# Performance work log

Measured on AMD Instinct MI355X. Metric: run time of the kernel, lower is better.

## Reference

```python
import jax, jax.numpy as jnp
import numpy as np

N, H, V, MAX_STEPS = 256, 128, 64, 4

def setup_inputs() -> dict:
    key = jax.random.key(0)
    ks = jax.random.split(key, 16)
    def w(k, shape, fan_in):
        return jax.random.normal(k, shape, dtype=jnp.float32) / np.sqrt(fan_in)
    inp = {}
    inp['node_embeddings'] = jax.random.normal(ks[0], (N, H), dtype=jnp.float32)
    inp['skip_embeddings'] = jax.random.normal(ks[1], (N, N, H), dtype=jnp.float32)
    inp['Wx'] = w(ks[2], (H, 4 * H), H)
    inp['Wh'] = w(ks[3], (H, 4 * H), H)
    inp['b'] = jnp.zeros((4 * H,), jnp.float32)
    inp['Wxs'] = w(ks[4], (H, 4 * H), H)
    inp['Whs'] = w(ks[5], (H, 4 * H), H)
    inp['bs'] = jnp.zeros((4 * H,), jnp.float32)
    inp['Wb'] = w(ks[6], (2 * H, 2), 2 * H)
    inp['bb'] = jnp.zeros((2,), jnp.float32)
    inp['Wk'] = w(ks[7], (H, H), H)
    inp['bk'] = jnp.zeros((H,), jnp.float32)
    inp['Wq'] = w(ks[8], (2 * H, H), 2 * H)
    inp['bq'] = jnp.zeros((H,), jnp.float32)
    inp['Wl'] = w(ks[9], (2 * H, 1), 2 * H)
    inp['bl'] = jnp.zeros((1,), jnp.float32)
    inp['Wd'] = w(ks[10], (2 * H, V), 2 * H)
    inp['bd'] = jnp.zeros((V,), jnp.float32)
    # valid skips only forward in the program (include diagonal = no-skip)
    inp['skip_mask'] = jnp.triu(jnp.ones((N, N), dtype=bool))
    inp['true_indexes'] = jax.random.randint(ks[11], (N,), 0, N, dtype=jnp.int32)
    inp['false_indexes'] = jax.random.randint(ks[12], (N,), 0, N, dtype=jnp.int32)
    inp['exit_index'] = N - 1
    return inp

def _lstm(c, h, x, Wx, Wh, b):
    gates = x @ Wx + h @ Wh + b  # [..., 4H]
    i, f, g, o = jnp.split(gates, 4, axis=-1)
    c2 = jax.nn.sigmoid(f) * c + jax.nn.sigmoid(i) * jnp.tanh(g)
    h2 = jax.nn.sigmoid(o) * jnp.tanh(c2)
    return c2, h2

def reference(node_embeddings, skip_embeddings, Wx, Wh, b, Wxs, Whs, bs,
              Wb, bb, Wk, bk, Wq, bq, Wl, bl, Wd, bd,
              skip_mask, true_indexes, false_indexes, exit_index):
    n, hdim = node_embeddings.shape
    eye = jnp.eye(n, dtype=node_embeddings.dtype)
    ip0 = jnp.zeros((n,), node_embeddings.dtype).at[0].set(1.0)
    c0 = jnp.zeros((n, hdim), node_embeddings.dtype)
    h0 = jnp.zeros((n, hdim), node_embeddings.dtype)
    keys = skip_embeddings @ Wk + bk  # [N,N,H] (input-only, precompute)

    def step(carry, _):
        ip, c, h = carry
        # per-node LSTM proposals
        c_p, h_p = _lstm(c, h, node_embeddings, Wx, Wh, b)  # [N,H]
        hid = jnp.concatenate([c_p, h_p], axis=-1)  # [N,2H]
        # skip proposals: carry of source i applied to skip embedding (i,j)
        c_sk, h_sk = _lstm(c[:, None, :], h[:, None, :], skip_embeddings, Wxs, Whs, bs)  # [N,N,H]
        # branch decisions
        branch = jax.nn.softmax(hid @ Wb + bb, axis=-1)  # [N,2]
        # skip decisions (per source i, softmax over destinations j)
        queries = hid @ Wq + bq  # [N,H]
        kq = jax.nn.relu(jnp.concatenate(
            [keys, jnp.broadcast_to(queries[:, None, :], (n, n, hdim))], axis=-1))  # [N,N,2H]
        logits = jnp.einsum('ijk,kl->ijl', kq, Wl)[..., 0] + bl[0]  # [N,N]
        skip_dec = jax.nn.softmax(jnp.where(skip_mask, logits, -jnp.inf), axis=-1)
        # aggregation (IPA)
        yes_skip = skip_dec * (1.0 - eye)  # zero diagonal
        no_skip = jnp.diagonal(skip_dec)
        p_bt = ip * no_skip * branch[:, 0]
        p_bf = ip * no_skip * branch[:, 1]
        new_ip = (jax.ops.segment_sum(p_bt, true_indexes, num_segments=n)
                  + jax.ops.segment_sum(p_bf, false_indexes, num_segments=n)
                  + jnp.einsum('i,ij->j', ip, yes_skip))
        denom = new_ip[:, None] + 1e-7
        def agg(hp, hsk):
            t = jax.ops.segment_sum(hp * p_bt[:, None], true_indexes, num_segments=n)
            f = jax.ops.segment_sum(hp * p_bf[:, None], false_indexes, num_segments=n)
            s = jnp.einsum('ijh,i,ij->jh', hsk, ip, yes_skip)
            return (t + f + s) / denom
        return (new_ip, agg(c_p, c_sk), agg(h_p, h_sk)), None

    (ip, c, h), _ = jax.lax.scan(step, (ip0, c0, h0), None, length=MAX_STEPS)
    exit_concat = jnp.concatenate([c[exit_index], h[exit_index]], axis=-1)  # [2H]
    return exit_concat @ Wd + bd  # [V]
```

## Files before the change

### kernel.cpp

```cpp
#include <hip/hip_runtime.h>
#include <hip/hip_bf16.h>

constexpr int NN = 256;
constexpr int HH = 128;
constexpr int GG = 512;
constexpr int NP = NN * NN;

typedef __attribute__((ext_vector_type(8))) short short8;
typedef __attribute__((ext_vector_type(4))) float f32x4;

__device__ unsigned short g_xs[(size_t)NP * GG];
__device__ unsigned short g_wfr[20 * 512 * 8];
__device__ float g_bsp[GG];
__device__ float g_pwh[HH * GG];
__device__ float g_pws[HH * GG];
__device__ float g_kterm[NP];
__device__ float g_yeswT[NP];
__device__ float g_noskip[NN];
__device__ float g_xg[NN * GG];
__device__ float g_xga[NN * GG];
__device__ float g_hws[NN * GG];
__device__ float g_c[NN * HH];
__device__ float g_h[NN * HH];
__device__ float g_sc[NN * HH];
__device__ float g_sh[NN * HH];
__device__ float g_ip[NN];
__device__ float g_nip[NN];

__device__ __forceinline__ unsigned short f2bf(float f) {
  unsigned int u = __float_as_uint(f);
  u = (u + 0x7fffu + ((u >> 16) & 1u)) >> 16;
  return (unsigned short)u;
}
__device__ __forceinline__ float bf2f(unsigned short s) {
  return __uint_as_float(((unsigned int)s) << 16);
}
__device__ __forceinline__ float frcp(float x) {
#if __has_builtin(__builtin_amdgcn_rcpf)
  return __builtin_amdgcn_rcpf(x);
#else
  return 1.0f / x;
#endif
}
__device__ __forceinline__ float sigm(float x) { return frcp(1.f + __expf(-x)); }
__device__ __forceinline__ float tanhfast(float x) { return 1.f - 2.f * frcp(__expf(2.f * x) + 1.f); }

__global__ __launch_bounds__(512) void k_pre(const float* __restrict__ NE,
                                             const float* __restrict__ Wx,
                                             const float* __restrict__ b,
                                             const float* __restrict__ Wxs,
                                             const float* __restrict__ Wk,
                                             const float* __restrict__ bs,
                                             const float* __restrict__ Wh,
                                             const float* __restrict__ Whs) {
  const int bid = blockIdx.x;
  const int tid = threadIdx.x;
  if (bid < 64) {
    const int idx = bid * 512 + tid;
    g_sc[idx] = 0.f; g_sh[idx] = 0.f; g_c[idx] = 0.f; g_h[idx] = 0.f;
    *(float4*)&g_hws[(size_t)idx * 4] = make_float4(0.f, 0.f, 0.f, 0.f);
    if (idx < NN) { g_nip[idx] = 0.f; g_ip[idx] = (idx == 0) ? 1.f : 0.f; }
  } else if (bid < 84) {
    const int bidx = bid - 64;
    const int tile = bidx >> 2, ks = bidx & 3;
    const int ct = tid >> 6, l = tid & 63;
    const int c = ct * 16 + (l & 15);
    const int kbase = ks * 32 + (l >> 4) * 8;
    int src = 0;
    if (tile < 4) src = (c & 3) * 128 + tile * 32 + (c >> 2);
    unsigned short* dst = &g_wfr[((size_t)bidx * 512 + tid) * 8];
#pragma unroll
    for (int e = 0; e < 8; ++e) {
      int k = kbase + e;
      float v = (tile < 4) ? Wxs[k * GG + src] : Wk[k * HH + c];
      dst[e] = f2bf(v);
    }
    if (tile < 4 && ks == 0 && (l >> 4) == 0) g_bsp[tile * 128 + c] = bs[src];
  } else if (bid < 116) {
    const int k = (bid - 84) * 4 + (tid >> 7), t = tid & 127;
    float4 a = make_float4(Wh[k * GG + t], Wh[k * GG + 128 + t], Wh[k * GG + 256 + t], Wh[k * GG + 384 + t]);
    float4 s = make_float4(Whs[k * GG + t], Whs[k * GG + 128 + t], Whs[k * GG + 256 + t], Whs[k * GG + 384 + t]);
    *(float4*)&g_pwh[((size_t)k * HH + t) * 4] = a;
    *(float4*)&g_pws[((size_t)k * HH + t) * 4] = s;
  } else {
    __shared__ float ne[4][HH];
    const int sub = tid >> 7, t = tid & 127;
    const int i = (bid - 116) * 4 + sub;
    ne[sub][t] = NE[i * HH + t];
    __syncthreads();
    float a0 = b[t], a1 = b[128 + t], a2 = b[256 + t], a3 = b[384 + t];
    for (int k = 0; k < HH; ++k) {
      float x = ne[sub][k];
      a0 = fmaf(x, Wx[k * GG + t], a0);
      a1 = fmaf(x, Wx[k * GG + 128 + t], a1);
      a2 = fmaf(x, Wx[k * GG + 256 + t], a2);
      a3 = fmaf(x, Wx[k * GG + 384 + t], a3);
    }
    float4 v = make_float4(a0, a1, a2, a3);
    *(float4*)&g_xg[((size_t)i * HH + t) * 4] = v;
    *(float4*)&g_xga[((size_t)i * HH + t) * 4] = v;
  }
}

__device__ __forceinline__ void loadB(short8* dst, int tile, int ks, int l) {
  const unsigned short* wf = &g_wfr[((size_t)(tile * 4 + ks)) * 4096 + l * 8];
#pragma unroll
  for (int ct = 0; ct < 8; ++ct) dst[ct] = *(const short8*)(wf + ct * 512);
}

__global__ __launch_bounds__(256) void k_gemm(const float* __restrict__ SE,
                                              const float* __restrict__ bk,
                                              const float* __restrict__ Wl) {
  __shared__ __align__(16) char lds[32768];
  const int bid = blockIdx.x;
  const int xcd = bid & 7;
  const int w = bid >> 3;
  const int x = (w / 5) * 8 + xcd;
  const int tile = w % 5;
  const int pb = (x < 128) ? (x * 2) : ((x - 128) * 2 + 1);
  const int pairBase = pb * 128;
  const int tid = threadIdx.x;

  for (int cc = tid; cc < 2048; cc += 256) {
    int row = cc >> 4, kc = cc & 15;
    const float* src = SE + (size_t)(pairBase + row) * HH + kc * 8;
    float4 f0 = *(const float4*)(src);
    float4 f1 = *(const float4*)(src + 4);
    short8 v;
    v[0] = (short)f2bf(f0.x); v[1] = (short)f2bf(f0.y); v[2] = (short)f2bf(f0.z); v[3] = (short)f2bf(f0.w);
    v[4] = (short)f2bf(f1.x); v[5] = (short)f2bf(f1.y); v[6] = (short)f2bf(f1.z); v[7] = (short)f2bf(f1.w);
    *(short8*)(lds + row * 256 + ((kc * 16) ^ ((row & 7) << 4))) = v;
  }
  __syncthreads();

  const int wv = tid >> 6;
  const int l = tid & 63;
  const int l15 = l & 15, lg = l >> 4;

  f32x4 acc[2][8];
#pragma unroll
  for (int rt = 0; rt < 2; ++rt)
#pragma unroll
    for (int ct = 0; ct < 8; ++ct) acc[rt][ct] = (f32x4){0.f, 0.f, 0.f, 0.f};

  short8 bA[8], bB[8];
  loadB(bA, tile, 0, l);
#pragma unroll
  for (int ks = 0; ks < 4; ks += 2) {
    loadB(bB, tile, ks + 1, l);
    {
      const int kb = ks * 64 + lg * 16;
      short8 a[2];
#pragma unroll
      for (int rt = 0; rt < 2; ++rt) {
        int row = wv * 32 + rt * 16 + l15;
        a[rt] = *(const short8*)(lds + row * 256 + (kb ^ ((row & 7) << 4)));
      }
#pragma unroll
      for (int rt = 0; rt < 2; ++rt)
#pragma unroll
        for (int ct = 0; ct < 8; ++ct)
          acc[rt][ct] = __builtin_amdgcn_mfma_f32_16x16x32_bf16(a[rt], bA[ct], acc[rt][ct], 0, 0, 0);
    }
    if (ks + 2 < 4) loadB(bA, tile, ks + 2, l);
    {
      const int kb = (ks + 1) * 64 + lg * 16;
      short8 a[2];
#pragma unroll
      for (int rt = 0; rt < 2; ++rt) {
        int row = wv * 32 + rt * 16 + l15;
        a[rt] = *(const short8*)(lds + row * 256 + (kb ^ ((row & 7) << 4)));
      }
#pragma unroll
      for (int rt = 0; rt < 2; ++rt)
#pragma unroll
        for (int ct = 0; ct < 8; ++ct)
          acc[rt][ct] = __builtin_amdgcn_mfma_f32_16x16x32_bf16(a[rt], bB[ct], acc[rt][ct], 0, 0, 0);
    }
  }

  if (tile < 4) {
#pragma unroll
    for (int rt = 0; rt < 2; ++rt)
#pragma unroll
      for (int ct = 0; ct < 8; ++ct) {
        const int col = ct * 16 + l15;
        const float bsv = g_bsp[tile * 128 + col];
#pragma unroll
        for (int r = 0; r < 4; ++r) {
          int row = wv * 32 + rt * 16 + lg * 4 + r;
          int pair = pairBase + row;
          int jj = pair & 255, ii = pair >> 8;
          if (jj > ii)
            g_xs[((size_t)jj * NN + ii) * GG + tile * 128 + col] = f2bf(acc[rt][ct][r] + bsv);
        }
      }
  } else {
#pragma unroll
    for (int rt = 0; rt < 2; ++rt) {
#pragma unroll
      for (int r = 0; r < 4; ++r) {
        float s = 0.f;
#pragma unroll
        for (int ct = 0; ct < 8; ++ct) {
          int col = ct * 16 + l15;
          float x2 = acc[rt][ct][r] + bk[col];
          x2 = fmaxf(x2, 0.f);
          s = fmaf(x2, Wl[col], s);
        }
#pragma unroll
        for (int m = 1; m < 16; m <<= 1) s += __shfl_xor(s, m, 64);
        int row = wv * 32 + rt * 16 + lg * 4 + r;
        int pair = pairBase + row;
        int jj = pair & 255, ii = pair >> 8;
        if (l15 == 0 && jj >= ii) g_kterm[pair] = s;
      }
    }
  }
}

__global__ __launch_bounds__(256) void k_softmax() {
  const int i = blockIdx.x, j = threadIdx.x;
  __shared__ float sm[NN];
  float x = -1e30f;
  if (j >= i) x = g_kterm[i * NN + j];
  sm[j] = x;
  __syncthreads();
  for (int s = 128; s > 0; s >>= 1) { if (j < s) sm[j] = fmaxf(sm[j], sm[j + s]); __syncthreads(); }
  float mx = sm[0];
  __syncthreads();
  float e = (j >= i) ? __expf(x - mx) : 0.f;
  sm[j] = e;
  __syncthreads();
  for (int s = 128; s > 0; s >>= 1) { if (j < s) sm[j] += sm[j + s]; __syncthreads(); }
  float p = e * frcp(sm[0]);
  g_yeswT[j * NN + i] = (j == i) ? 0.f : p;
  if (j == i) g_noskip[i] = p;
}

__global__ __launch_bounds__(128) void k_step(const float* __restrict__ Wb,
                                              const float* __restrict__ bb,
                                              const int* __restrict__ tix,
                                              const int* __restrict__ fix) {
  const int t = threadIdx.x;
  if (blockIdx.x < 256) {
    const int i = blockIdx.x;
    const float ipi = g_ip[i];
    if (ipi == 0.f) return;
    __shared__ float red[2][2];
    const float4 a = *(const float4*)&g_xga[((size_t)i * HH + t) * 4];
    float co = g_c[i * HH + t];
    float c2 = sigm(a.y) * co + sigm(a.x) * tanhfast(a.z);
    float h2 = sigm(a.w) * tanhfast(c2);
    float q0 = c2 * Wb[2 * t] + h2 * Wb[2 * (128 + t)];
    float q1 = c2 * Wb[2 * t + 1] + h2 * Wb[2 * (128 + t) + 1];
#pragma unroll
    for (int m = 1; m < 64; m <<= 1) { q0 += __shfl_xor(q0, m, 64); q1 += __shfl_xor(q1, m, 64); }
    if ((t & 63) == 0) { red[t >> 6][0] = q0; red[t >> 6][1] = q1; }
    __syncthreads();
    float l0 = red[0][0] + red[1][0] + bb[0];
    float l1 = red[0][1] + red[1][1] + bb[1];
    float mm = fmaxf(l0, l1);
    float e0 = __expf(l0 - mm), e1 = __expf(l1 - mm);
    float inv = frcp(e0 + e1);
    float ipv = ipi * g_noskip[i];
    if (ipv != 0.f) {
      float pbt = ipv * e0 * inv, pbf = ipv * e1 * inv;
      int ti = tix[i], fi = fix[i];
      atomicAdd(&g_sc[ti * HH + t], c2 * pbt);
      atomicAdd(&g_sh[ti * HH + t], h2 * pbt);
      atomicAdd(&g_sc[fi * HH + t], c2 * pbf);
      atomicAdd(&g_sh[fi * HH + t], h2 * pbf);
      if (t == 0) { atomicAdd(&g_nip[ti], pbt); atomicAdd(&g_nip[fi], pbf); }
    }
  } else {
    const int idx = blockIdx.x - 256;
    const int j = idx >> 4, ch = idx & 15;
    const int i0 = ch * 16;
    if (i0 >= j) return;
    const int iN = (j - i0 < 16) ? (j - i0) : 16;
    __shared__ float wsh[16];
    if (t < 16) wsh[t] = (t < iN) ? g_ip[i0 + t] * g_yeswT[j * NN + i0 + t] : 0.f;
    __syncthreads();
    float s16 = 0.f;
#pragma unroll
    for (int q = 0; q < 16; ++q) s16 += wsh[q];
    if (s16 == 0.f) return;
    float accC = 0.f, accH = 0.f, accW = 0.f;
    for (int ii = 0; ii < iN; ++ii) {
      const float wgt = wsh[ii];
      const int i = i0 + ii;
      const ushort4 gv = *(const ushort4*)&g_xs[((size_t)j * NN + i) * GG + t * 4];
      float4 hw = *(const float4*)&g_hws[((size_t)i * HH + t) * 4];
      float xi = bf2f(gv.x) + hw.x;
      float xf = bf2f(gv.y) + hw.y;
      float xg = bf2f(gv.z) + hw.z;
      float xo = bf2f(gv.w) + hw.w;
      float c2 = sigm(xf) * g_c[i * HH + t] + sigm(xi) * tanhfast(xg);
      float h2 = sigm(xo) * tanhfast(c2);
      accC = fmaf(wgt, c2, accC);
      accH = fmaf(wgt, h2, accH);
      accW += wgt;
    }
    atomicAdd(&g_sc[j * HH + t], accC);
    atomicAdd(&g_sh[j * HH + t], accH);
    if (t == 0) atomicAdd(&g_nip[j], accW);
  }
}

__global__ __launch_bounds__(256) void k_finish(const int last,
                                                const float* __restrict__ Wd,
                                                const float* __restrict__ bd,
                                                const int* __restrict__ ei,
                                                float* __restrict__ out) {
  const int j0 = blockIdx.x * 4;
  const int tid = threadIdx.x;
  __shared__ float hsm[4][HH];
  __shared__ float nipsh[4];
  if (tid < 4) {
    const int j = j0 + tid;
    float nip = g_nip[j];
    nipsh[tid] = nip;
    g_ip[j] = nip;
    g_nip[j] = 0.f;
  }
  __syncthreads();
#pragma unroll
  for (int s = 0; s < 2; ++s) {
    const int slot = tid + s * 256;
    const int jj = slot >> 7, t = slot & 127;
    const int j = j0 + jj;
    float d = frcp(nipsh[jj] + 1e-7f);
    float cv = g_sc[j * HH + t] * d;
    float hv = g_sh[j * HH + t] * d;
    g_c[j * HH + t] = cv;
    g_h[j * HH + t] = hv;
    hsm[jj][t] = hv;
    g_sc[j * HH + t] = 0.f;
    g_sh[j * HH + t] = 0.f;
  }
  __syncthreads();
  if (last) {
    const int e = ei[0];
    if (e >= j0 && e < j0 + 4 && tid < 64) {
      const int v = tid;
      float sacc = bd[v];
      const float* cc = &g_c[e * HH];
      const float* hh = &g_h[e * HH];
      for (int h = 0; h < HH; ++h) {
        sacc = fmaf(cc[h], Wd[h * 64 + v], sacc);
        sacc = fmaf(hh[h], Wd[(128 + h) * 64 + v], sacc);
      }
      out[v] = sacc;
    }
    return;
  }
  const int m = tid >> 7, t = tid & 127;
  const float* __restrict__ W = m ? g_pws : g_pwh;
  float4 a0 = make_float4(0.f, 0.f, 0.f, 0.f), a1 = a0, a2 = a0, a3 = a0;
#pragma unroll 4
  for (int k = 0; k < HH; ++k) {
    const float4 w = *(const float4*)&W[((size_t)k * HH + t) * 4];
    const float h0 = hsm[0][k], h1 = hsm[1][k], h2 = hsm[2][k], h3 = hsm[3][k];
    a0.x = fmaf(h0, w.x, a0.x); a0.y = fmaf(h0, w.y, a0.y); a0.z = fmaf(h0, w.z, a0.z); a0.w = fmaf(h0, w.w, a0.w);
    a1.x = fmaf(h1, w.x, a1.x); a1.y = fmaf(h1, w.y, a1.y); a1.z = fmaf(h1, w.z, a1.z); a1.w = fmaf(h1, w.w, a1.w);
    a2.x = fmaf(h2, w.x, a2.x); a2.y = fmaf(h2, w.y, a2.y); a2.z = fmaf(h2, w.z, a2.z); a2.w = fmaf(h2, w.w, a2.w);
    a3.x = fmaf(h3, w.x, a3.x); a3.y = fmaf(h3, w.y, a3.y); a3.z = fmaf(h3, w.z, a3.z); a3.w = fmaf(h3, w.w, a3.w);
  }
  if (m == 0) {
    float4 x0 = *(const float4*)&g_xg[((size_t)(j0 + 0) * HH + t) * 4];
    float4 x1 = *(const float4*)&g_xg[((size_t)(j0 + 1) * HH + t) * 4];
    float4 x2 = *(const float4*)&g_xg[((size_t)(j0 + 2) * HH + t) * 4];
    float4 x3 = *(const float4*)&g_xg[((size_t)(j0 + 3) * HH + t) * 4];
    *(float4*)&g_xga[((size_t)(j0 + 0) * HH + t) * 4] = make_float4(x0.x + a0.x, x0.y + a0.y, x0.z + a0.z, x0.w + a0.w);
    *(float4*)&g_xga[((size_t)(j0 + 1) * HH + t) * 4] = make_float4(x1.x + a1.x, x1.y + a1.y, x1.z + a1.z, x1.w + a1.w);
    *(float4*)&g_xga[((size_t)(j0 + 2) * HH + t) * 4] = make_float4(x2.x + a2.x, x2.y + a2.y, x2.z + a2.z, x2.w + a2.w);
    *(float4*)&g_xga[((size_t)(j0 + 3) * HH + t) * 4] = make_float4(x3.x + a3.x, x3.y + a3.y, x3.z + a3.z, x3.w + a3.w);
  } else {
    *(float4*)&g_hws[((size_t)(j0 + 0) * HH + t) * 4] = a0;
    *(float4*)&g_hws[((size_t)(j0 + 1) * HH + t) * 4] = a1;
    *(float4*)&g_hws[((size_t)(j0 + 2) * HH + t) * 4] = a2;
    *(float4*)&g_hws[((size_t)(j0 + 3) * HH + t) * 4] = a3;
  }
}

extern "C" void kernel_launch(void* const* d_in, const int* in_sizes, int n_in,
                              void* d_out, int out_size, void* d_ws, size_t ws_size,
                              hipStream_t stream) {
  const float* NE  = (const float*)d_in[0];
  const float* SE  = (const float*)d_in[1];
  const float* Wx  = (const float*)d_in[2];
  const float* Wh  = (const float*)d_in[3];
  const float* b   = (const float*)d_in[4];
  const float* Wxs = (const float*)d_in[5];
  const float* Whs = (const float*)d_in[6];
  const float* bs  = (const float*)d_in[7];
  const float* Wb  = (const float*)d_in[8];
  const float* bb  = (const float*)d_in[9];
  const float* Wk  = (const float*)d_in[10];
  const float* bk  = (const float*)d_in[11];
  const float* Wl  = (const float*)d_in[14];
  const float* Wd  = (const float*)d_in[16];
  const float* bd  = (const float*)d_in[17];
  const int* tix = (const int*)d_in[19];
  const int* fix = (const int*)d_in[20];
  const int* ei  = (const int*)d_in[21];
  float* out = (float*)d_out;

  k_pre<<<180, 512, 0, stream>>>(NE, Wx, b, Wxs, Wk, bs, Wh, Whs);
  k_gemm<<<1920, 256, 0, stream>>>(SE, bk, Wl);
  k_softmax<<<256, 256, 0, stream>>>();
  for (int s = 0; s < 4; ++s) {
    k_step<<<256 + NN * 16, 128, 0, stream>>>(Wb, bb, tix, fix);
    k_finish<<<64, 256, 0, stream>>>(s == 3, Wd, bd, ei, out);
  }
}
```

Before: 159.6 us.

## Pre-convert skip embeddings to bf16 once and double-buffer GEMM tiles via direct-to-LDS loads

Extra blocks in k_pre convert skip_embeddings from fp32 to bf16 once, writing them to a global buffer already in the swizzled layout. Before, each of the five column-tile GEMM blocks re-read and re-converted the same fp32 rows. k_gemm becomes a 96x5 grid in which each block loops over four row tiles. Each tile is staged into double-buffered LDS with global_load_lds, so the next tile's load overlaps MFMA work on the current one. The cost is an extra 16 MB global write plus reread, 64 KB of LDS per block, and fewer blocks, which lowers occupancy.

```diff
diff --git a/kernel.cpp b/kernel.cpp
--- a/kernel.cpp
+++ b/kernel.cpp
@@ -10,6 +10,7 @@
 typedef __attribute__((ext_vector_type(4))) float f32x4;
 
 __device__ unsigned short g_xs[(size_t)NP * GG];
+__device__ unsigned short g_sebf[(size_t)NP * HH];
 __device__ unsigned short g_wfr[20 * 512 * 8];
 __device__ float g_bsp[GG];
 __device__ float g_pwh[HH * GG];
@@ -52,7 +53,8 @@
                                              const float* __restrict__ Wk,
                                              const float* __restrict__ bs,
                                              const float* __restrict__ Wh,
-                                             const float* __restrict__ Whs) {
+                                             const float* __restrict__ Whs,
+                                             const float* __restrict__ SE) {
   const int bid = blockIdx.x;
   const int tid = threadIdx.x;
   if (bid < 64) {
@@ -82,7 +84,7 @@
     float4 s = make_float4(Whs[k * GG + t], Whs[k * GG + 128 + t], Whs[k * GG + 256 + t], Whs[k * GG + 384 + t]);
     *(float4*)&g_pwh[((size_t)k * HH + t) * 4] = a;
     *(float4*)&g_pws[((size_t)k * HH + t) * 4] = s;
-  } else {
+  } else if (bid < 180) {
     __shared__ float ne[4][HH];
     const int sub = tid >> 7, t = tid & 127;
     const int i = (bid - 116) * 4 + sub;
@@ -99,6 +101,20 @@
     float4 v = make_float4(a0, a1, a2, a3);
     *(float4*)&g_xg[((size_t)i * HH + t) * 4] = v;
     *(float4*)&g_xga[((size_t)i * HH + t) * 4] = v;
+  } else {
+    const int p0 = (bid - 180) * 256;
+    for (int e = tid; e < 4096; e += 512) {
+      const int pl = e >> 4, g = e & 15;
+      const int pair = p0 + pl;
+      const int gs = g ^ (pair & 7);
+      const float* src = SE + (size_t)pair * HH + gs * 8;
+      float4 f0 = *(const float4*)(src);
+      float4 f1 = *(const float4*)(src + 4);
+      short8 v;
+      v[0] = (short)f2bf(f0.x); v[1] = (short)f2bf(f0.y); v[2] = (short)f2bf(f0.z); v[3] = (short)f2bf(f0.w);
+      v[4] = (short)f2bf(f1.x); v[5] = (short)f2bf(f1.y); v[6] = (short)f2bf(f1.z); v[7] = (short)f2bf(f1.w);
+      *(short8*)&g_sebf[(size_t)pair * HH + g * 8] = v;
+    }
   }
 }
 
@@ -108,114 +124,126 @@
   for (int ct = 0; ct < 8; ++ct) dst[ct] = *(const short8*)(wf + ct * 512);
 }
 
-__global__ __launch_bounds__(256) void k_gemm(const float* __restrict__ SE,
-                                              const float* __restrict__ bk,
+__global__ __launch_bounds__(256) void k_gemm(const float* __restrict__ bk,
                                               const float* __restrict__ Wl) {
-  __shared__ __align__(16) char lds[32768];
-  const int bid = blockIdx.x;
-  const int xcd = bid & 7;
-  const int w = bid >> 3;
-  const int x = (w / 5) * 8 + xcd;
-  const int tile = w % 5;
-  const int pb = (x < 128) ? (x * 2) : ((x - 128) * 2 + 1);
-  const int pairBase = pb * 128;
+  __shared__ __align__(16) char lds[65536];
+  const int tile = blockIdx.y;
   const int tid = threadIdx.x;
-
-  for (int cc = tid; cc < 2048; cc += 256) {
-    int row = cc >> 4, kc = cc & 15;
-    const float* src = SE + (size_t)(pairBase + row) * HH + kc * 8;
-    float4 f0 = *(const float4*)(src);
-    float4 f1 = *(const float4*)(src + 4);
-    short8 v;
-    v[0] = (short)f2bf(f0.x); v[1] = (short)f2bf(f0.y); v[2] = (short)f2bf(f0.z); v[3] = (short)f2bf(f0.w);
-    v[4] = (short)f2bf(f1.x); v[5] = (short)f2bf(f1.y); v[6] = (short)f2bf(f1.z); v[7] = (short)f2bf(f1.w);
-    *(short8*)(lds + row * 256 + ((kc * 16) ^ ((row & 7) << 4))) = v;
-  }
-  __syncthreads();
-
   const int wv = tid >> 6;
   const int l = tid & 63;
   const int l15 = l & 15, lg = l >> 4;
 
-  f32x4 acc[2][8];
-#pragma unroll
-  for (int rt = 0; rt < 2; ++rt)
-#pragma unroll
-    for (int ct = 0; ct < 8; ++ct) acc[rt][ct] = (f32x4){0.f, 0.f, 0.f, 0.f};
-
-  short8 bA[8], bB[8];
-  loadB(bA, tile, 0, l);
-#pragma unroll
-  for (int ks = 0; ks < 4; ks += 2) {
-    loadB(bB, tile, ks + 1, l);
-    {
-      const int kb = ks * 64 + lg * 16;
-      short8 a[2];
+  auto stage = [&](int buf, int q) {
+    const int x = blockIdx.x * 4 + q;
+    const int pb = (x < 128) ? (x * 2) : ((x - 128) * 2 + 1);
+    const char* src = (const char*)g_sebf + (size_t)pb * 128 * 256;
+    char* dstb = lds + buf * 32768 + wv * 1024;
+#pragma unroll
+    for (int it = 0; it < 8; ++it) {
+      __builtin_amdgcn_global_load_lds(
+          (const __attribute__((address_space(1))) unsigned int*)(src + it * 4096 + tid * 16),
+          (__attribute__((address_space(3))) unsigned int*)(dstb + it * 4096),
+          16, 0, 0);
+    }
+  };
+
+  stage(0, 0);
+  asm volatile("s_waitcnt vmcnt(0)" ::: "memory");
+  __builtin_amdgcn_s_barrier();
+
+  int cur = 0;
+  for (int q = 0; q < 4; ++q) {
+    if (q < 3) stage(cur ^ 1, q + 1);
+
+    const char* abuf = lds + cur * 32768;
+    const int x = blockIdx.x * 4 + q;
+    const int pb = (x < 128) ? (x * 2) : ((x - 128) * 2 + 1);
+    const int pairBase = pb * 128;
+
+    f32x4 acc[2][8];
+#pragma unroll
+    for (int rt = 0; rt < 2; ++rt)
+#pragma unroll
+      for (int ct = 0; ct < 8; ++ct) acc[rt][ct] = (f32x4){0.f, 0.f, 0.f, 0.f};
+
+    short8 bA[8], bB[8];
+    loadB(bA, tile, 0, l);
+#pragma unroll
+    for (int ks = 0; ks < 4; ks += 2) {
+      loadB(bB, tile, ks + 1, l);
+      {
+        const int kb = ks * 64 + lg * 16;
+        short8 a[2];
+#pragma unroll
+        for (int rt = 0; rt < 2; ++rt) {
+          int row = wv * 32 + rt * 16 + l15;
+          a[rt] = *(const short8*)(abuf + row * 256 + (kb ^ ((row & 7) << 4)));
+        }
+#pragma unroll
+        for (int rt = 0; rt < 2; ++rt)
+#pragma unroll
+          for (int ct = 0; ct < 8; ++ct)
+            acc[rt][ct] = __builtin_amdgcn_mfma_f32_16x16x32_bf16(a[rt], bA[ct], acc[rt][ct], 0, 0, 0);
+      }
+      if (ks + 2 < 4) loadB(bA, tile, ks + 2, l);
+      {
+        const int kb = (ks + 1) * 64 + lg * 16;
+        short8 a[2];
+#pragma unroll
+        for (int rt = 0; rt < 2; ++rt) {
+          int row = wv * 32 + rt * 16 + l15;
+          a[rt] = *(const short8*)(abuf + row * 256 + (kb ^ ((row & 7) << 4)));
+        }
+#pragma unroll
+        for (int rt = 0; rt < 2; ++rt)
+#pragma unroll
+          for (int ct = 0; ct < 8; ++ct)
+            acc[rt][ct] = __builtin_amdgcn_mfma_f32_16x16x32_bf16(a[rt], bB[ct], acc[rt][ct], 0, 0, 0);
+      }
+    }
+
+    if (tile < 4) {
+#pragma unroll
+      for (int rt = 0; rt < 2; ++rt)
+#pragma unroll
+        for (int ct = 0; ct < 8; ++ct) {
+          const int col = ct * 16 + l15;
+          const float bsv = g_bsp[tile * 128 + col];
+#pragma unroll
+          for (int r = 0; r < 4; ++r) {
+            int row = wv * 32 + rt * 16 + lg * 4 + r;
+            int pair = pairBase + row;
+            int jj = pair & 255, ii = pair >> 8;
+            if (jj > ii)
+              g_xs[((size_t)jj * NN + ii) * GG + tile * 128 + col] = f2bf(acc[rt][ct][r] + bsv);
+          }
+        }
+    } else {
 #pragma unroll
       for (int rt = 0; rt < 2; ++rt) {
-        int row = wv * 32 + rt * 16 + l15;
-        a[rt] = *(const short8*)(lds + row * 256 + (kb ^ ((row & 7) << 4)));
-      }
-#pragma unroll
-      for (int rt = 0; rt < 2; ++rt)
-#pragma unroll
-        for (int ct = 0; ct < 8; ++ct)
-          acc[rt][ct] = __builtin_amdgcn_mfma_f32_16x16x32_bf16(a[rt], bA[ct], acc[rt][ct], 0, 0, 0);
-    }
-    if (ks + 2 < 4) loadB(bA, tile, ks + 2, l);
-    {
-      const int kb = (ks + 1) * 64 + lg * 16;
-      short8 a[2];
-#pragma unroll
-      for (int rt = 0; rt < 2; ++rt) {
-        int row = wv * 32 + rt * 16 + l15;
-        a[rt] = *(const short8*)(lds + row * 256 + (kb ^ ((row & 7) << 4)));
-      }
-#pragma unroll
-      for (int rt = 0; rt < 2; ++rt)
-#pragma unroll
-        for (int ct = 0; ct < 8; ++ct)
-          acc[rt][ct] = __builtin_amdgcn_mfma_f32_16x16x32_bf16(a[rt], bB[ct], acc[rt][ct], 0, 0, 0);
-    }
-  }
-
-  if (tile < 4) {
-#pragma unroll
-    for (int rt = 0; rt < 2; ++rt)
-#pragma unroll
-      for (int ct = 0; ct < 8; ++ct) {
-        const int col = ct * 16 + l15;
-        const float bsv = g_bsp[tile * 128 + col];
 #pragma unroll
         for (int r = 0; r < 4; ++r) {
+          float s = 0.f;
+#pragma unroll
+          for (int ct = 0; ct < 8; ++ct) {
+            int col = ct * 16 + l15;
+            float x2 = acc[rt][ct][r] + bk[col];
+            x2 = fmaxf(x2, 0.f);
+            s = fmaf(x2, Wl[col], s);
+          }
+#pragma unroll
+          for (int m = 1; m < 16; m <<= 1) s += __shfl_xor(s, m, 64);
           int row = wv * 32 + rt * 16 + lg * 4 + r;
           int pair = pairBase + row;
           int jj = pair & 255, ii = pair >> 8;
-          if (jj > ii)
-            g_xs[((size_t)jj * NN + ii) * GG + tile * 128 + col] = f2bf(acc[rt][ct][r] + bsv);
+          if (l15 == 0 && jj >= ii) g_kterm[pair] = s;
         }
       }
-  } else {
-#pragma unroll
-    for (int rt = 0; rt < 2; ++rt) {
-#pragma unroll
-      for (int r = 0; r < 4; ++r) {
-        float s = 0.f;
-#pragma unroll
-        for (int ct = 0; ct < 8; ++ct) {
-          int col = ct * 16 + l15;
-          float x2 = acc[rt][ct][r] + bk[col];
-          x2 = fmaxf(x2, 0.f);
-          s = fmaf(x2, Wl[col], s);
-        }
-#pragma unroll
-        for (int m = 1; m < 16; m <<= 1) s += __shfl_xor(s, m, 64);
-        int row = wv * 32 + rt * 16 + lg * 4 + r;
-        int pair = pairBase + row;
-        int jj = pair & 255, ii = pair >> 8;
-        if (l15 == 0 && jj >= ii) g_kterm[pair] = s;
-      }
-    }
+    }
+
+    asm volatile("s_waitcnt vmcnt(0)" ::: "memory");
+    __builtin_amdgcn_s_barrier();
+    cur ^= 1;
   }
 }
 
@@ -407,8 +435,8 @@
   const int* ei  = (const int*)d_in[21];
   float* out = (float*)d_out;
 
-  k_pre<<<180, 512, 0, stream>>>(NE, Wx, b, Wxs, Wk, bs, Wh, Whs);
-  k_gemm<<<1920, 256, 0, stream>>>(SE, bk, Wl);
+  k_pre<<<436, 512, 0, stream>>>(NE, Wx, b, Wxs, Wk, bs, Wh, Whs, SE);
+  k_gemm<<<dim3(96, 5), 256, 0, stream>>>(bk, Wl);
   k_softmax<<<256, 256, 0, stream>>>();
   for (int s = 0; s < 4; ++s) {
     k_step<<<256 + NN * 16, 128, 0, stream>>>(Wb, bb, tix, fix);
```

New measurement: 167.5 us. +4.9%, slower.
